# Performance work log

Hardware: AMD Instinct MI355X
Metric: run time of the kernel (lower is better)

The kernel has to match this reference:

```python
import jax, jax.numpy as jnp
import numpy as np

EMB_DIM = 1024
N_HEADS = 16
HEAD_DIM = EMB_DIM // N_HEADS


def setup_inputs() -> dict:
    key = jax.random.key(0)
    ks = jax.random.split(key, 6)
    B, S, D = 2, 2048, EMB_DIM
    s = 1.0 / np.sqrt(D)
    return {
        "x": jax.random.normal(ks[0], (B, S, D), dtype=jnp.float32),
        "wq": jax.random.normal(ks[1], (D, D), dtype=jnp.float32) * s,
        "wk": jax.random.normal(ks[2], (D, D), dtype=jnp.float32) * s,
        "wv": jax.random.normal(ks[3], (D, D), dtype=jnp.float32) * s,
        "wo": jax.random.normal(ks[4], (D, D), dtype=jnp.float32) * s,
        "bo": jax.random.normal(ks[5], (D,), dtype=jnp.float32) * 0.01,
    }


def reference(x, wq, wk, wv, wo, bo):
    B, S, D = x.shape
    H, Hd = N_HEADS, HEAD_DIM
    # projections (torch Linear: y = x @ W.T; here weights are stored as [in, out])
    q = (x @ wq).reshape(B, S, H, Hd).transpose(0, 2, 1, 3)  # [B,H,S,Hd]
    k = (x @ wk).reshape(B, S, H, Hd).transpose(0, 2, 1, 3)
    v = (x @ wv).reshape(B, S, H, Hd).transpose(0, 2, 1, 3)
    scores = jnp.einsum("bhqd,bhkd->bhqk", q, k)  # [B,H,S,S]
    causal = jnp.tril(jnp.ones((S, S), dtype=bool))  # keep lower triangle
    scores = jnp.where(causal, scores, -jnp.inf)
    weights = jax.nn.softmax(scores / np.sqrt(Hd), axis=-1)
    ctx = jnp.einsum("bhqk,bhkd->bhqd", weights, v)  # [B,H,S,Hd]
    ctx = ctx.transpose(0, 2, 1, 3).reshape(B, S, D)
    return ctx @ wo + bo
```

## Files before the change

### kernel.cpp

```cpp
#include <hip/hip_runtime.h>
#include <hip/hip_bf16.h>

constexpr int B = 2, S = 2048, D = 1024, H = 16, Hd = 64;
constexpr int M = B * S;
constexpr int K = 1024;

typedef __attribute__((ext_vector_type(8))) short short8;
typedef __attribute__((ext_vector_type(4))) float f32x4;

#if __has_builtin(__builtin_amdgcn_exp2f)
#define EXP2F __builtin_amdgcn_exp2f
#else
#define EXP2F exp2f
#endif

__device__ __forceinline__ float bf2f(unsigned short u) {
    return __uint_as_float(((unsigned)u) << 16);
}
__device__ __forceinline__ unsigned short f2bf(float f) {
    unsigned u = __float_as_uint(f);
    u += 0x7FFF + ((u >> 16) & 1);
    return (unsigned short)(u >> 16);
}
__device__ __forceinline__ void gload_lds16(const unsigned short* g, unsigned short* l) {
    __builtin_amdgcn_global_load_lds(
        (const __attribute__((address_space(1))) void*)g,
        (__attribute__((address_space(3))) void*)l, 16, 0, 0);
}

__global__ __launch_bounds__(256) void prep_kernel(
    const float* __restrict__ x,
    const float* __restrict__ wq, const float* __restrict__ wk,
    const float* __restrict__ wv, const float* __restrict__ wo,
    unsigned short* __restrict__ xb,
    unsigned short* __restrict__ wqkv_t, unsigned short* __restrict__ wo_t)
{
    __shared__ float tile[64][65];
    const int z = blockIdx.z;
    const int t = threadIdx.x;
    if (z == 4) {
        const int bid = blockIdx.y * 16 + blockIdx.x;
        const size_t base_i = ((size_t)bid * 256 + t) * 8;
        #pragma unroll
        for (int it = 0; it < 8; ++it) {
            const size_t i = base_i + (size_t)it * 524288;
            float4 a = *(const float4*)(x + i), b = *(const float4*)(x + i + 4);
            ushort4 u0 = {f2bf(a.x), f2bf(a.y), f2bf(a.z), f2bf(a.w)};
            ushort4 u1 = {f2bf(b.x), f2bf(b.y), f2bf(b.z), f2bf(b.w)};
            *(ushort4*)(xb + i) = u0;
            *(ushort4*)(xb + i + 4) = u1;
        }
        return;
    }
    const float* w = (z == 0) ? wq : (z == 1) ? wk : (z == 2) ? wv : wo;
    unsigned short* dst = (z == 3) ? wo_t : wqkv_t + (size_t)z * K * K;
    const int k0 = blockIdx.x * 64, n0 = blockIdx.y * 64;
    #pragma unroll
    for (int it = 0; it < 16; ++it) {
        int idx = t + it * 256;
        tile[idx >> 6][idx & 63] = w[(size_t)(k0 + (idx >> 6)) * K + n0 + (idx & 63)];
    }
    __syncthreads();
    #pragma unroll
    for (int it = 0; it < 16; ++it) {
        int idx = t + it * 256;
        int r = idx >> 6, c = idx & 63;
        dst[(size_t)(n0 + r) * K + k0 + c] = f2bf(tile[c][r]);
    }
}

__global__ __launch_bounds__(256) void qkv_mfma_kernel(
    const unsigned short* __restrict__ xa, const unsigned short* __restrict__ bt,
    unsigned short* __restrict__ q, unsigned short* __restrict__ k,
    unsigned short* __restrict__ vt)
{
    __shared__ unsigned short A_lds[128][32];
    __shared__ unsigned short B_lds[128][32];
    const int t = threadIdx.x, w = t >> 6, l = t & 63;
    const int lr = l & 15, lg = l >> 4;
    const int wm = w >> 1, wn = w & 1;
    const int m0 = blockIdx.x * 128, n0 = blockIdx.y * 128;
    const int srow = l >> 2;
    const int skofs = (((l & 3) ^ ((l >> 2) & 3))) * 8;
    const int rslot = (lg ^ (lr & 3)) * 8;

    f32x4 acc[4][4];
    #pragma unroll
    for (int i = 0; i < 4; ++i)
        #pragma unroll
        for (int j = 0; j < 4; ++j) acc[i][j] = (f32x4){0.f, 0.f, 0.f, 0.f};

    for (int k0 = 0; k0 < K; k0 += 32) {
        #pragma unroll
        for (int p = 0; p < 2; ++p) {
            const int c = w * 2 + p;
            gload_lds16(xa + (size_t)(m0 + c * 16 + srow) * K + k0 + skofs, &A_lds[c * 16][0]);
            gload_lds16(bt + (size_t)(n0 + c * 16 + srow) * K + k0 + skofs, &B_lds[c * 16][0]);
        }
        __syncthreads();
        short8 af[4], bf[4];
        #pragma unroll
        for (int i = 0; i < 4; ++i) af[i] = *(const short8*)&A_lds[wm * 64 + i * 16 + lr][rslot];
        #pragma unroll
        for (int j = 0; j < 4; ++j) bf[j] = *(const short8*)&B_lds[wn * 64 + j * 16 + lr][rslot];
        #pragma unroll
        for (int i = 0; i < 4; ++i)
            #pragma unroll
            for (int j = 0; j < 4; ++j)
                acc[i][j] = __builtin_amdgcn_mfma_f32_16x16x32_bf16(af[i], bf[j], acc[i][j], 0, 0, 0);
        __syncthreads();
    }

    const int z = (n0 >> 10);
    const float scale = (z == 0) ? 0.125f * 1.44269504f : 1.0f;
    #pragma unroll
    for (int i = 0; i < 4; ++i) {
        const int mbase = m0 + wm * 64 + i * 16 + lg * 4;
        #pragma unroll
        for (int j = 0; j < 4; ++j) {
            const int n = n0 + wn * 64 + j * 16 + lr;
            const int nn = n & 1023, hh = nn >> 6, hd = nn & 63;
            #pragma unroll
            for (int r = 0; r < 4; ++r) {
                const int mm = mbase + r, bb = mm >> 11, ss = mm & (S - 1);
                const unsigned short val = f2bf(acc[i][j][r] * scale);
                if (z == 0)      q[((size_t)(bb * H + hh) * S + ss) * Hd + hd] = val;
                else if (z == 1) k[((size_t)(bb * H + hh) * S + ss) * Hd + hd] = val;
                else             vt[((size_t)(bb * H + hh) * Hd + hd) * S + ss] = val;
            }
        }
    }
}

__global__ __launch_bounds__(256) void out_mfma_kernel(
    const unsigned short* __restrict__ a, const unsigned short* __restrict__ bt,
    const float* __restrict__ bias, float* __restrict__ out)
{
    __shared__ unsigned short A_lds[128][32];
    __shared__ unsigned short B_lds[128][32];
    const int t = threadIdx.x, w = t >> 6, l = t & 63;
    const int lr = l & 15, lg = l >> 4;
    const int wm = w >> 1, wn = w & 1;
    const int m0 = blockIdx.x * 128, n0 = blockIdx.y * 128;
    const int srow = l >> 2;
    const int skofs = (((l & 3) ^ ((l >> 2) & 3))) * 8;
    const int rslot = (lg ^ (lr & 3)) * 8;

    f32x4 acc[4][4];
    #pragma unroll
    for (int i = 0; i < 4; ++i)
        #pragma unroll
        for (int j = 0; j < 4; ++j) acc[i][j] = (f32x4){0.f, 0.f, 0.f, 0.f};

    for (int k0 = 0; k0 < K; k0 += 32) {
        #pragma unroll
        for (int p = 0; p < 2; ++p) {
            const int c = w * 2 + p;
            gload_lds16(a  + (size_t)(m0 + c * 16 + srow) * K + k0 + skofs, &A_lds[c * 16][0]);
            gload_lds16(bt + (size_t)(n0 + c * 16 + srow) * K + k0 + skofs, &B_lds[c * 16][0]);
        }
        __syncthreads();
        short8 af[4], bf[4];
        #pragma unroll
        for (int i = 0; i < 4; ++i) af[i] = *(const short8*)&A_lds[wm * 64 + i * 16 + lr][rslot];
        #pragma unroll
        for (int j = 0; j < 4; ++j) bf[j] = *(const short8*)&B_lds[wn * 64 + j * 16 + lr][rslot];
        #pragma unroll
        for (int i = 0; i < 4; ++i)
            #pragma unroll
            for (int j = 0; j < 4; ++j)
                acc[i][j] = __builtin_amdgcn_mfma_f32_16x16x32_bf16(af[i], bf[j], acc[i][j], 0, 0, 0);
        __syncthreads();
    }

    #pragma unroll
    for (int i = 0; i < 4; ++i) {
        const int mbase = m0 + wm * 64 + i * 16 + lg * 4;
        #pragma unroll
        for (int j = 0; j < 4; ++j) {
            const int n = n0 + wn * 64 + j * 16 + lr;
            const float bv = bias[n];
            #pragma unroll
            for (int r = 0; r < 4; ++r)
                out[(size_t)(mbase + r) * D + n] = acc[i][j][r] + bv;
        }
    }
}

__global__ __launch_bounds__(256) void attn_mfma_kernel(
    const unsigned short* __restrict__ q, const unsigned short* __restrict__ k,
    const unsigned short* __restrict__ vt, unsigned short* __restrict__ ctx)
{
    __shared__ unsigned short Kb[2][64 * 64];
    __shared__ unsigned short Vb[2][64 * 64];
    __shared__ unsigned short P_lds[4][16 * 64];
    const int t = threadIdx.x, w = t >> 6, l = t & 63;
    const int lr = l & 15, lg = l >> 4;

    const int bid = blockIdx.x;
    const int xcd = bid & 7;
    const int j   = bid >> 3;
    const int m   = j >> 5;
    const int c0  = j & 31;
    const int bh  = xcd * 4 + m;
    const int bb  = bh >> 4, hh = bh & 15;
    const int cc  = (c0 + ((m >> 1) ? 8 : 0)) & 31;
    const int qt  = (m & 1) ? (31 - cc) : cc;

    const int q0 = qt * 64 + w * 16;
    const int diag = qt;
    const size_t base  = (size_t)(bb * H + hh) * S * Hd;
    const size_t vbase = (size_t)(bb * H + hh) * Hd * S;
    const int pswz = (lr & 7) << 3;

    const int srow0 = w * 16 + (l >> 3);
    const int scol  = (l & 7) * 8;

    short8 qf[2];
    #pragma unroll
    for (int ci = 0; ci < 2; ++ci)
        qf[ci] = *(const short8*)(q + base + (size_t)(q0 + lr) * Hd + ci * 32 + lg * 8);

    f32x4 accO[4];
    #pragma unroll
    for (int hb = 0; hb < 4; ++hb) accO[hb] = (f32x4){0.f, 0.f, 0.f, 0.f};
    float l_part = 0.f;

    {
        short8 k0r[2], v0r[2];
        #pragma unroll
        for (int it = 0; it < 2; ++it) {
            const int row = srow0 + it * 8;
            k0r[it] = *(const short8*)(k + base + (size_t)row * Hd + scol);
            v0r[it] = *(const short8*)(vt + vbase + (size_t)row * S + scol);
        }
        #pragma unroll
        for (int it = 0; it < 2; ++it) {
            const int row = srow0 + it * 8;
            const int wc = (scol ^ ((row & 7) * 8));
            *(short8*)&Kb[0][row * 64 + wc] = k0r[it];
            *(short8*)&Vb[0][row * 64 + wc] = v0r[it];
        }
    }
    __syncthreads();

    int cur = 0;
    for (int kt = 0; kt < diag; ++kt) {
        short8 nK[2], nV[2];
        {
            const unsigned short* kg = k + base + (size_t)(kt + 1) * 64 * Hd;
            const unsigned short* vg = vt + vbase + (size_t)(kt + 1) * 64;
            #pragma unroll
            for (int it = 0; it < 2; ++it) {
                const int row = srow0 + it * 8;
                nK[it] = *(const short8*)(kg + (size_t)row * Hd + scol);
                nV[it] = *(const short8*)(vg + (size_t)row * S + scol);
            }
        }

        const unsigned short* Kc = Kb[cur];
        const unsigned short* Vc = Vb[cur];

        f32x4 accS[4];
        __builtin_amdgcn_s_setprio(1);
        #pragma unroll
        for (int kc = 0; kc < 4; ++kc) {
            accS[kc] = (f32x4){0.f, 0.f, 0.f, 0.f};
            const int krow = kc * 16 + lr;
            #pragma unroll
            for (int ci = 0; ci < 2; ++ci) {
                short8 kf = *(const short8*)&Kc[krow * 64 +
                    ((ci * 32 + lg * 8) ^ ((krow & 7) * 8))];
                accS[kc] = __builtin_amdgcn_mfma_f32_16x16x32_bf16(kf, qf[ci], accS[kc], 0, 0, 0);
            }
        }
        __builtin_amdgcn_s_setprio(0);

        float ps[16];
        #pragma unroll
        for (int i = 0; i < 16; ++i)
            ps[i] = EXP2F(accS[i >> 2][i & 3] - 16.f);
        float s8[8];
        #pragma unroll
        for (int i = 0; i < 8; ++i) s8[i] = ps[i] + ps[i + 8];
        l_part += ((s8[0] + s8[4]) + (s8[1] + s8[5])) +
                  ((s8[2] + s8[6]) + (s8[3] + s8[7]));

        #pragma unroll
        for (int kc = 0; kc < 4; ++kc) {
            uint2 pk;
            *(__hip_bfloat162*)&pk.x =
                __float22bfloat162_rn(make_float2(ps[kc * 4 + 0], ps[kc * 4 + 1]));
            *(__hip_bfloat162*)&pk.y =
                __float22bfloat162_rn(make_float2(ps[kc * 4 + 2], ps[kc * 4 + 3]));
            *(uint2*)&P_lds[w][lr * 64 + ((kc * 16 + lg * 4) ^ pswz)] = pk;
        }
        short8 pa[2];
        #pragma unroll
        for (int ci = 0; ci < 2; ++ci)
            pa[ci] = *(const short8*)&P_lds[w][lr * 64 + ((ci * 32 + lg * 8) ^ pswz)];

        __builtin_amdgcn_s_setprio(1);
        #pragma unroll
        for (int hb = 0; hb < 4; ++hb) {
            const int vrow = hb * 16 + lr;
            #pragma unroll
            for (int ci = 0; ci < 2; ++ci) {
                short8 vf = *(const short8*)&Vc[vrow * 64 +
                    ((ci * 32 + lg * 8) ^ ((vrow & 7) * 8))];
                accO[hb] = __builtin_amdgcn_mfma_f32_16x16x32_bf16(vf, pa[ci], accO[hb], 0, 0, 0);
            }
        }
        __builtin_amdgcn_s_setprio(0);

        #pragma unroll
        for (int it = 0; it < 2; ++it) {
            const int row = srow0 + it * 8;
            const int wc = (scol ^ ((row & 7) * 8));
            *(short8*)&Kb[cur ^ 1][row * 64 + wc] = nK[it];
            *(short8*)&Vb[cur ^ 1][row * 64 + wc] = nV[it];
        }
        __syncthreads();
        cur ^= 1;
    }

    {
        const unsigned short* Kc = Kb[cur];
        const unsigned short* Vc = Vb[cur];
        f32x4 accS[4];
        __builtin_amdgcn_s_setprio(1);
        #pragma unroll
        for (int kc = 0; kc < 4; ++kc) {
            accS[kc] = (f32x4){0.f, 0.f, 0.f, 0.f};
            const int krow = kc * 16 + lr;
            #pragma unroll
            for (int ci = 0; ci < 2; ++ci) {
                short8 kf = *(const short8*)&Kc[krow * 64 +
                    ((ci * 32 + lg * 8) ^ ((krow & 7) * 8))];
                accS[kc] = __builtin_amdgcn_mfma_f32_16x16x32_bf16(kf, qf[ci], accS[kc], 0, 0, 0);
            }
        }
        __builtin_amdgcn_s_setprio(0);

        float ps[16];
        #pragma unroll
        for (int kc = 0; kc < 4; ++kc)
            #pragma unroll
            for (int r = 0; r < 4; ++r) {
                float s = accS[kc][r];
                if (kc * 16 + lg * 4 + r > w * 16 + lr) s = -INFINITY;
                ps[kc * 4 + r] = EXP2F(s - 16.f);
            }
        float s8[8];
        #pragma unroll
        for (int i = 0; i < 8; ++i) s8[i] = ps[i] + ps[i + 8];
        l_part += ((s8[0] + s8[4]) + (s8[1] + s8[5])) +
                  ((s8[2] + s8[6]) + (s8[3] + s8[7]));

        #pragma unroll
        for (int kc = 0; kc < 4; ++kc) {
            uint2 pk;
            *(__hip_bfloat162*)&pk.x =
                __float22bfloat162_rn(make_float2(ps[kc * 4 + 0], ps[kc * 4 + 1]));
            *(__hip_bfloat162*)&pk.y =
                __float22bfloat162_rn(make_float2(ps[kc * 4 + 2], ps[kc * 4 + 3]));
            *(uint2*)&P_lds[w][lr * 64 + ((kc * 16 + lg * 4) ^ pswz)] = pk;
        }
        short8 pa[2];
        #pragma unroll
        for (int ci = 0; ci < 2; ++ci)
            pa[ci] = *(const short8*)&P_lds[w][lr * 64 + ((ci * 32 + lg * 8) ^ pswz)];

        __builtin_amdgcn_s_setprio(1);
        #pragma unroll
        for (int hb = 0; hb < 4; ++hb) {
            const int vrow = hb * 16 + lr;
            #pragma unroll
            for (int ci = 0; ci < 2; ++ci) {
                short8 vf = *(const short8*)&Vc[vrow * 64 +
                    ((ci * 32 + lg * 8) ^ ((vrow & 7) * 8))];
                accO[hb] = __builtin_amdgcn_mfma_f32_16x16x32_bf16(vf, pa[ci], accO[hb], 0, 0, 0);
            }
        }
        __builtin_amdgcn_s_setprio(0);
    }

    float l_run = l_part;
    l_run += __shfl_xor(l_run, 16);
    l_run += __shfl_xor(l_run, 32);
    const float inv = 1.f / l_run;
    unsigned short* crow = ctx + (size_t)(bb * S + q0 + lr) * D + hh * Hd + lg * 4;
    #pragma unroll
    for (int hb = 0; hb < 4; ++hb) {
        ushort4 o;
        o.x = f2bf(accO[hb][0] * inv);
        o.y = f2bf(accO[hb][1] * inv);
        o.z = f2bf(accO[hb][2] * inv);
        o.w = f2bf(accO[hb][3] * inv);
        *(ushort4*)(crow + hb * 16) = o;
    }
}

extern "C" void kernel_launch(void* const* d_in, const int* in_sizes, int n_in,
                              void* d_out, int out_size, void* d_ws, size_t ws_size,
                              hipStream_t stream) {
    const float* x  = (const float*)d_in[0];
    const float* wq = (const float*)d_in[1];
    const float* wk = (const float*)d_in[2];
    const float* wv = (const float*)d_in[3];
    const float* wo = (const float*)d_in[4];
    const float* bo = (const float*)d_in[5];
    float* out = (float*)d_out;

    char* ws = (char*)d_ws;
    unsigned short* x_bf   = (unsigned short*)ws;
    unsigned short* q      = (unsigned short*)(ws + ((size_t)8  << 20));
    unsigned short* kk     = (unsigned short*)(ws + ((size_t)16 << 20));
    unsigned short* vt     = (unsigned short*)(ws + ((size_t)24 << 20));
    unsigned short* ctx    = x_bf;
    unsigned short* wqkv_t = (unsigned short*)(ws + ((size_t)32 << 20));
    unsigned short* wo_t   = (unsigned short*)(ws + ((size_t)38 << 20));

    dim3 gprep(16, 16, 5);
    prep_kernel<<<gprep, 256, 0, stream>>>(x, wq, wk, wv, wo, x_bf, wqkv_t, wo_t);

    dim3 gqkv(M / 128, 3072 / 128);
    qkv_mfma_kernel<<<gqkv, 256, 0, stream>>>(x_bf, wqkv_t, q, kk, vt);

    attn_mfma_kernel<<<1024, 256, 0, stream>>>(q, kk, vt, ctx);

    dim3 gout(M / 128, D / 128);
    out_mfma_kernel<<<gout, 256, 0, stream>>>(ctx, wo_t, bo, out);
}
```

Before: 110.9 us.

## Split attention KV range across two wave pairs per 32-row query tile

Each block now handles 32 query rows instead of 64. The four waves split into two query strips times two KV halves, and each half streams its own K/V tiles through its own LDS buffer. Partial O and row sums from the second half are reduced through LDS before the normalized output is written. The grid doubles to 2048 blocks and tiles are scheduled longest-first, aiming for better balance and parallelism on the causal triangle. In exchange, the double buffering is lost, there are two barriers per iteration, and idle waves on the odd tile count waste some slots.

```diff
diff --git a/kernel.cpp b/kernel.cpp
--- a/kernel.cpp
+++ b/kernel.cpp
@@ -196,30 +196,30 @@
     __shared__ unsigned short P_lds[4][16 * 64];
     const int t = threadIdx.x, w = t >> 6, l = t & 63;
     const int lr = l & 15, lg = l >> 4;
+    const int strip = w & 1, s = w >> 1;
 
     const int bid = blockIdx.x;
     const int xcd = bid & 7;
-    const int j   = bid >> 3;
-    const int m   = j >> 5;
-    const int c0  = j & 31;
-    const int bh  = xcd * 4 + m;
+    const int u   = bid >> 3;
+    const int m2  = u >> 6;
+    const int bh  = xcd * 4 + m2;
     const int bb  = bh >> 4, hh = bh & 15;
-    const int cc  = (c0 + ((m >> 1) ? 8 : 0)) & 31;
-    const int qt  = (m & 1) ? (31 - cc) : cc;
-
-    const int q0 = qt * 64 + w * 16;
-    const int diag = qt;
+    const int j   = 63 - (u & 63);
+    const int T   = (j >> 1) + 1;
+    const int c0  = (T + 1) >> 1;
+
     const size_t base  = (size_t)(bb * H + hh) * S * Hd;
     const size_t vbase = (size_t)(bb * H + hh) * Hd * S;
     const int pswz = (lr & 7) << 3;
 
-    const int srow0 = w * 16 + (l >> 3);
+    const int srow0 = strip * 32 + (l >> 3);
     const int scol  = (l & 7) * 8;
 
+    const int qrow0 = j * 32 + strip * 16;
     short8 qf[2];
     #pragma unroll
     for (int ci = 0; ci < 2; ++ci)
-        qf[ci] = *(const short8*)(q + base + (size_t)(q0 + lr) * Hd + ci * 32 + lg * 8);
+        qf[ci] = *(const short8*)(q + base + (size_t)(qrow0 + lr) * Hd + ci * 32 + lg * 8);
 
     f32x4 accO[4];
     #pragma unroll
@@ -227,177 +227,158 @@
     float l_part = 0.f;
 
     {
-        short8 k0r[2], v0r[2];
-        #pragma unroll
-        for (int it = 0; it < 2; ++it) {
-            const int row = srow0 + it * 8;
-            k0r[it] = *(const short8*)(k + base + (size_t)row * Hd + scol);
-            v0r[it] = *(const short8*)(vt + vbase + (size_t)row * S + scol);
-        }
-        #pragma unroll
-        for (int it = 0; it < 2; ++it) {
-            const int row = srow0 + it * 8;
-            const int wc = (scol ^ ((row & 7) * 8));
-            *(short8*)&Kb[0][row * 64 + wc] = k0r[it];
-            *(short8*)&Vb[0][row * 64 + wc] = v0r[it];
+        const int pro = s ? c0 : 0;
+        if (!s || c0 < T) {
+            const unsigned short* kg = k + base + (size_t)pro * 64 * Hd;
+            const unsigned short* vg = vt + vbase + (size_t)pro * 64;
+            short8 pK[4], pV[4];
+            #pragma unroll
+            for (int it = 0; it < 4; ++it) {
+                const int row = srow0 + it * 8;
+                pK[it] = *(const short8*)(kg + (size_t)row * Hd + scol);
+                pV[it] = *(const short8*)(vg + (size_t)row * S + scol);
+            }
+            #pragma unroll
+            for (int it = 0; it < 4; ++it) {
+                const int row = srow0 + it * 8;
+                const int wc = (scol ^ ((row & 7) * 8));
+                *(short8*)&Kb[s][row * 64 + wc] = pK[it];
+                *(short8*)&Vb[s][row * 64 + wc] = pV[it];
+            }
         }
     }
     __syncthreads();
 
-    int cur = 0;
-    for (int kt = 0; kt < diag; ++kt) {
-        short8 nK[2], nV[2];
-        {
-            const unsigned short* kg = k + base + (size_t)(kt + 1) * 64 * Hd;
-            const unsigned short* vg = vt + vbase + (size_t)(kt + 1) * 64;
-            #pragma unroll
-            for (int it = 0; it < 2; ++it) {
-                const int row = srow0 + it * 8;
-                nK[it] = *(const short8*)(kg + (size_t)row * Hd + scol);
-                nV[it] = *(const short8*)(vg + (size_t)row * S + scol);
-            }
-        }
-
-        const unsigned short* Kc = Kb[cur];
-        const unsigned short* Vc = Vb[cur];
-
-        f32x4 accS[4];
-        __builtin_amdgcn_s_setprio(1);
-        #pragma unroll
-        for (int kc = 0; kc < 4; ++kc) {
-            accS[kc] = (f32x4){0.f, 0.f, 0.f, 0.f};
-            const int krow = kc * 16 + lr;
-            #pragma unroll
-            for (int ci = 0; ci < 2; ++ci) {
-                short8 kf = *(const short8*)&Kc[krow * 64 +
-                    ((ci * 32 + lg * 8) ^ ((krow & 7) * 8))];
-                accS[kc] = __builtin_amdgcn_mfma_f32_16x16x32_bf16(kf, qf[ci], accS[kc], 0, 0, 0);
-            }
-        }
-        __builtin_amdgcn_s_setprio(0);
-
-        float ps[16];
-        #pragma unroll
-        for (int i = 0; i < 16; ++i)
-            ps[i] = EXP2F(accS[i >> 2][i & 3] - 16.f);
-        float s8[8];
-        #pragma unroll
-        for (int i = 0; i < 8; ++i) s8[i] = ps[i] + ps[i + 8];
-        l_part += ((s8[0] + s8[4]) + (s8[1] + s8[5])) +
-                  ((s8[2] + s8[6]) + (s8[3] + s8[7]));
-
-        #pragma unroll
-        for (int kc = 0; kc < 4; ++kc) {
-            uint2 pk;
-            *(__hip_bfloat162*)&pk.x =
-                __float22bfloat162_rn(make_float2(ps[kc * 4 + 0], ps[kc * 4 + 1]));
-            *(__hip_bfloat162*)&pk.y =
-                __float22bfloat162_rn(make_float2(ps[kc * 4 + 2], ps[kc * 4 + 3]));
-            *(uint2*)&P_lds[w][lr * 64 + ((kc * 16 + lg * 4) ^ pswz)] = pk;
-        }
-        short8 pa[2];
-        #pragma unroll
-        for (int ci = 0; ci < 2; ++ci)
-            pa[ci] = *(const short8*)&P_lds[w][lr * 64 + ((ci * 32 + lg * 8) ^ pswz)];
-
-        __builtin_amdgcn_s_setprio(1);
+    for (int it = 0; it < c0; ++it) {
+        const int mt = s ? (c0 + it) : it;
+        const bool active  = (mt < T);
+        const bool st_act  = s ? (mt + 1 < T) : (mt + 1 < c0);
+
+        short8 nK[4], nV[4];
+        if (st_act) {
+            const unsigned short* kg = k + base + (size_t)(mt + 1) * 64 * Hd;
+            const unsigned short* vg = vt + vbase + (size_t)(mt + 1) * 64;
+            #pragma unroll
+            for (int c2 = 0; c2 < 4; ++c2) {
+                const int row = srow0 + c2 * 8;
+                nK[c2] = *(const short8*)(kg + (size_t)row * Hd + scol);
+                nV[c2] = *(const short8*)(vg + (size_t)row * S + scol);
+            }
+        }
+
+        if (active) {
+            const unsigned short* Kc = Kb[s];
+            const unsigned short* Vc = Vb[s];
+
+            f32x4 accS[4];
+            __builtin_amdgcn_s_setprio(1);
+            #pragma unroll
+            for (int kc = 0; kc < 4; ++kc) {
+                accS[kc] = (f32x4){0.f, 0.f, 0.f, 0.f};
+                const int krow = kc * 16 + lr;
+                #pragma unroll
+                for (int ci = 0; ci < 2; ++ci) {
+                    short8 kf = *(const short8*)&Kc[krow * 64 +
+                        ((ci * 32 + lg * 8) ^ ((krow & 7) * 8))];
+                    accS[kc] = __builtin_amdgcn_mfma_f32_16x16x32_bf16(kf, qf[ci], accS[kc], 0, 0, 0);
+                }
+            }
+            __builtin_amdgcn_s_setprio(0);
+
+            float ps[16];
+            if (mt == T - 1) {
+                const int qi = qrow0 + lr;
+                #pragma unroll
+                for (int kc = 0; kc < 4; ++kc)
+                    #pragma unroll
+                    for (int r = 0; r < 4; ++r) {
+                        float sv = accS[kc][r];
+                        if (mt * 64 + kc * 16 + lg * 4 + r > qi) sv = -INFINITY;
+                        ps[kc * 4 + r] = EXP2F(sv - 16.f);
+                    }
+            } else {
+                #pragma unroll
+                for (int i = 0; i < 16; ++i)
+                    ps[i] = EXP2F(accS[i >> 2][i & 3] - 16.f);
+            }
+            float s8[8];
+            #pragma unroll
+            for (int i = 0; i < 8; ++i) s8[i] = ps[i] + ps[i + 8];
+            l_part += ((s8[0] + s8[4]) + (s8[1] + s8[5])) +
+                      ((s8[2] + s8[6]) + (s8[3] + s8[7]));
+
+            #pragma unroll
+            for (int kc = 0; kc < 4; ++kc) {
+                uint2 pk;
+                *(__hip_bfloat162*)&pk.x =
+                    __float22bfloat162_rn(make_float2(ps[kc * 4 + 0], ps[kc * 4 + 1]));
+                *(__hip_bfloat162*)&pk.y =
+                    __float22bfloat162_rn(make_float2(ps[kc * 4 + 2], ps[kc * 4 + 3]));
+                *(uint2*)&P_lds[w][lr * 64 + ((kc * 16 + lg * 4) ^ pswz)] = pk;
+            }
+            short8 pa[2];
+            #pragma unroll
+            for (int ci = 0; ci < 2; ++ci)
+                pa[ci] = *(const short8*)&P_lds[w][lr * 64 + ((ci * 32 + lg * 8) ^ pswz)];
+
+            __builtin_amdgcn_s_setprio(1);
+            #pragma unroll
+            for (int hb = 0; hb < 4; ++hb) {
+                const int vrow = hb * 16 + lr;
+                #pragma unroll
+                for (int ci = 0; ci < 2; ++ci) {
+                    short8 vf = *(const short8*)&Vc[vrow * 64 +
+                        ((ci * 32 + lg * 8) ^ ((vrow & 7) * 8))];
+                    accO[hb] = __builtin_amdgcn_mfma_f32_16x16x32_bf16(vf, pa[ci], accO[hb], 0, 0, 0);
+                }
+            }
+            __builtin_amdgcn_s_setprio(0);
+        }
+
+        __syncthreads();
+        if (st_act) {
+            #pragma unroll
+            for (int c2 = 0; c2 < 4; ++c2) {
+                const int row = srow0 + c2 * 8;
+                const int wc = (scol ^ ((row & 7) * 8));
+                *(short8*)&Kb[s][row * 64 + wc] = nK[c2];
+                *(short8*)&Vb[s][row * 64 + wc] = nV[c2];
+            }
+        }
+        __syncthreads();
+    }
+
+    float* cb = (float*)&Kb[0][0];
+    float* blob = cb + (strip * 64 + l) * 17;
+    if (s == 1) {
+        #pragma unroll
+        for (int hb = 0; hb < 4; ++hb)
+            #pragma unroll
+            for (int r = 0; r < 4; ++r) blob[hb * 4 + r] = accO[hb][r];
+        blob[16] = l_part;
+    }
+    __syncthreads();
+    if (s == 0) {
+        #pragma unroll
+        for (int hb = 0; hb < 4; ++hb)
+            #pragma unroll
+            for (int r = 0; r < 4; ++r) accO[hb][r] += blob[hb * 4 + r];
+        l_part += blob[16];
+
+        float l_run = l_part;
+        l_run += __shfl_xor(l_run, 16);
+        l_run += __shfl_xor(l_run, 32);
+        const float inv = 1.f / l_run;
+        unsigned short* crow = ctx + (size_t)(bb * S + qrow0 + lr) * D + hh * Hd + lg * 4;
         #pragma unroll
         for (int hb = 0; hb < 4; ++hb) {
-            const int vrow = hb * 16 + lr;
-            #pragma unroll
-            for (int ci = 0; ci < 2; ++ci) {
-                short8 vf = *(const short8*)&Vc[vrow * 64 +
-                    ((ci * 32 + lg * 8) ^ ((vrow & 7) * 8))];
-                accO[hb] = __builtin_amdgcn_mfma_f32_16x16x32_bf16(vf, pa[ci], accO[hb], 0, 0, 0);
-            }
-        }
-        __builtin_amdgcn_s_setprio(0);
-
-        #pragma unroll
-        for (int it = 0; it < 2; ++it) {
-            const int row = srow0 + it * 8;
-            const int wc = (scol ^ ((row & 7) * 8));
-            *(short8*)&Kb[cur ^ 1][row * 64 + wc] = nK[it];
-            *(short8*)&Vb[cur ^ 1][row * 64 + wc] = nV[it];
-        }
-        __syncthreads();
-        cur ^= 1;
-    }
-
-    {
-        const unsigned short* Kc = Kb[cur];
-        const unsigned short* Vc = Vb[cur];
-        f32x4 accS[4];
-        __builtin_amdgcn_s_setprio(1);
-        #pragma unroll
-        for (int kc = 0; kc < 4; ++kc) {
-            accS[kc] = (f32x4){0.f, 0.f, 0.f, 0.f};
-            const int krow = kc * 16 + lr;
-            #pragma unroll
-            for (int ci = 0; ci < 2; ++ci) {
-                short8 kf = *(const short8*)&Kc[krow * 64 +
-                    ((ci * 32 + lg * 8) ^ ((krow & 7) * 8))];
-                accS[kc] = __builtin_amdgcn_mfma_f32_16x16x32_bf16(kf, qf[ci], accS[kc], 0, 0, 0);
-            }
-        }
-        __builtin_amdgcn_s_setprio(0);
-
-        float ps[16];
-        #pragma unroll
-        for (int kc = 0; kc < 4; ++kc)
-            #pragma unroll
-            for (int r = 0; r < 4; ++r) {
-                float s = accS[kc][r];
-                if (kc * 16 + lg * 4 + r > w * 16 + lr) s = -INFINITY;
-                ps[kc * 4 + r] = EXP2F(s - 16.f);
-            }
-        float s8[8];
-        #pragma unroll
-        for (int i = 0; i < 8; ++i) s8[i] = ps[i] + ps[i + 8];
-        l_part += ((s8[0] + s8[4]) + (s8[1] + s8[5])) +
-                  ((s8[2] + s8[6]) + (s8[3] + s8[7]));
-
-        #pragma unroll
-        for (int kc = 0; kc < 4; ++kc) {
-            uint2 pk;
-            *(__hip_bfloat162*)&pk.x =
-                __float22bfloat162_rn(make_float2(ps[kc * 4 + 0], ps[kc * 4 + 1]));
-            *(__hip_bfloat162*)&pk.y =
-                __float22bfloat162_rn(make_float2(ps[kc * 4 + 2], ps[kc * 4 + 3]));
-            *(uint2*)&P_lds[w][lr * 64 + ((kc * 16 + lg * 4) ^ pswz)] = pk;
-        }
-        short8 pa[2];
-        #pragma unroll
-        for (int ci = 0; ci < 2; ++ci)
-            pa[ci] = *(const short8*)&P_lds[w][lr * 64 + ((ci * 32 + lg * 8) ^ pswz)];
-
-        __builtin_amdgcn_s_setprio(1);
-        #pragma unroll
-        for (int hb = 0; hb < 4; ++hb) {
-            const int vrow = hb * 16 + lr;
-            #pragma unroll
-            for (int ci = 0; ci < 2; ++ci) {
-                short8 vf = *(const short8*)&Vc[vrow * 64 +
-                    ((ci * 32 + lg * 8) ^ ((vrow & 7) * 8))];
-                accO[hb] = __builtin_amdgcn_mfma_f32_16x16x32_bf16(vf, pa[ci], accO[hb], 0, 0, 0);
-            }
-        }
-        __builtin_amdgcn_s_setprio(0);
-    }
-
-    float l_run = l_part;
-    l_run += __shfl_xor(l_run, 16);
-    l_run += __shfl_xor(l_run, 32);
-    const float inv = 1.f / l_run;
-    unsigned short* crow = ctx + (size_t)(bb * S + q0 + lr) * D + hh * Hd + lg * 4;
-    #pragma unroll
-    for (int hb = 0; hb < 4; ++hb) {
-        ushort4 o;
-        o.x = f2bf(accO[hb][0] * inv);
-        o.y = f2bf(accO[hb][1] * inv);
-        o.z = f2bf(accO[hb][2] * inv);
-        o.w = f2bf(accO[hb][3] * inv);
-        *(ushort4*)(crow + hb * 16) = o;
+            ushort4 o;
+            o.x = f2bf(accO[hb][0] * inv);
+            o.y = f2bf(accO[hb][1] * inv);
+            o.z = f2bf(accO[hb][2] * inv);
+            o.w = f2bf(accO[hb][3] * inv);
+            *(ushort4*)(crow + hb * 16) = o;
+        }
     }
 }
 
@@ -427,7 +408,7 @@
     dim3 gqkv(M / 128, 3072 / 128);
     qkv_mfma_kernel<<<gqkv, 256, 0, stream>>>(x_bf, wqkv_t, q, kk, vt);
 
-    attn_mfma_kernel<<<1024, 256, 0, stream>>>(q, kk, vt, ctx);
+    attn_mfma_kernel<<<2048, 256, 0, stream>>>(q, kk, vt, ctx);
 
     dim3 gout(M / 128, D / 128);
     out_mfma_kernel<<<gout, 256, 0, stream>>>(ctx, wo_t, bo, out);
```

Measured after the change: 122.1 us. +10.1%, slower.
